# Performance work log

Measured on AMD Instinct MI355X. Metric: run time of the kernel, lower is better.

Reference implementation:

```python
import jax, jax.numpy as jnp
import numpy as np
from jax import lax

H = 39  # hidden size == input feature size (hardcoded in the torch module)


def _lstm_scan(xs, W_ih, W_hh, b_ih, b_hh):
    """Run a unidirectional LSTM over xs: (T, B, I) -> (T, B, H).
    PyTorch gate order: i, f, g, o."""
    T, B, _ = xs.shape
    # Precompute input projections for all timesteps: (T, B, 4H)
    pre = jnp.einsum('tbi,gi->tbg', xs, W_ih) + b_ih + b_hh
    h0 = jnp.zeros((B, H), dtype=xs.dtype)
    c0 = jnp.zeros((B, H), dtype=xs.dtype)

    def step(carry, g_in):
        h, c = carry
        g = g_in + h @ W_hh.T  # (B, 4H)
        i, f, gg, o = jnp.split(g, 4, axis=-1)
        i = jax.nn.sigmoid(i)
        f = jax.nn.sigmoid(f)
        gg = jnp.tanh(gg)
        o = jax.nn.sigmoid(o)
        c = f * c + i * gg
        h = o * jnp.tanh(c)
        return (h, c), h

    _, hs = lax.scan(step, (h0, c0), pre)
    return hs  # (T, B, H)


def setup_inputs() -> dict:
    key = jax.random.key(0)
    ks = jax.random.split(key, 9)
    B, T = 512, 2048
    s = 1.0 / np.sqrt(H)
    x = jax.random.normal(ks[0], (B, T * H), dtype=jnp.float32)
    def w(k, shape):
        return jax.random.uniform(k, shape, dtype=jnp.float32, minval=-s, maxval=s)
    return {
        'x': x,
        'W_ih_f': w(ks[1], (4 * H, H)),
        'W_hh_f': w(ks[2], (4 * H, H)),
        'b_ih_f': w(ks[3], (4 * H,)),
        'b_hh_f': w(ks[4], (4 * H,)),
        'W_ih_b': w(ks[5], (4 * H, H)),
        'W_hh_b': w(ks[6], (4 * H, H)),
        'b_ih_b': w(ks[7], (4 * H,)),
        'b_hh_b': w(ks[8], (4 * H,)),
    }


def reference(x, W_ih_f, W_hh_f, b_ih_f, b_hh_f, W_ih_b, W_hh_b, b_ih_b, b_hh_b):
    B = x.shape[0]
    T = x.shape[1] // H
    xs = jnp.swapaxes(x.reshape(B, T, H), 0, 1)  # (T, B, H)

    h_f = _lstm_scan(xs, W_ih_f, W_hh_f, b_ih_f, b_hh_f)          # forward dir, time order
    h_b_rev = _lstm_scan(xs[::-1], W_ih_b, W_hh_b, b_ih_b, b_hh_b)  # backward dir, processing order
    # torch output for backward dir is h_b_rev flipped to time order; the module then
    # flips it again along time before concat -> equals h_b_rev directly.
    out = jnp.concatenate([h_f, h_b_rev], axis=-1)  # (T, B, 2H)
    out = jnp.swapaxes(out, 0, 1).reshape(B, T * 2 * H)
    return out
```

## Files before the change

### kernel.cpp

```cpp
#include <hip/hip_runtime.h>
#include <math.h>

#define H   39
#define G4  156
#define TL  2048
#define BB  512

__device__ __forceinline__ float sigmoid_f(float x) {
    return 1.0f / (1.0f + __expf(-x));
}

__device__ __forceinline__ float tanh_f(float x) {
    float a = fabsf(x);
    float e = __expf(2.0f * a);
    float t = 1.0f - 2.0f / (e + 1.0f);
    return copysignf(t, x);
}

__global__ __launch_bounds__(192, 3)
void lstm_bidir_kernel(const float* __restrict__ x,
                       const float* __restrict__ W_ih_f, const float* __restrict__ W_hh_f,
                       const float* __restrict__ b_ih_f, const float* __restrict__ b_hh_f,
                       const float* __restrict__ W_ih_b, const float* __restrict__ W_hh_b,
                       const float* __restrict__ b_ih_b, const float* __restrict__ b_hh_b,
                       float* __restrict__ out)
{
    const int blk = blockIdx.x;
    const int b   = blk >> 1;
    const int dir = blk & 1;
    const int j   = threadIdx.x;

    const float* W_ih = dir ? W_ih_b : W_ih_f;
    const float* W_hh = dir ? W_hh_b : W_hh_f;
    const float* b_ih = dir ? b_ih_b : b_ih_f;
    const float* b_hh = dir ? b_hh_b : b_hh_f;

    __shared__ float h_buf[40];
    __shared__ float x_buf[40];
    __shared__ float gates[G4];

    float wih[H], whh[H];
    float bias = 0.0f;
    if (j < G4) {
        #pragma unroll
        for (int k = 0; k < H; ++k) {
            wih[k] = W_ih[j * H + k];
            whh[k] = W_hh[j * H + k];
        }
        bias = b_ih[j] + b_hh[j];
    }

    const float* xrow = x + (size_t)b * (TL * H);
    float* orow = out + (size_t)b * (TL * 2 * H) + dir * H;

    float c = 0.0f;
    if (j < H) {
        h_buf[j] = 0.0f;
        const int t0 = dir ? (TL - 1) : 0;
        x_buf[j] = xrow[t0 * H + j];
    }
    __syncthreads();

    for (int s = 0; s < TL; ++s) {
        float xnext = 0.0f;
        if (j < H && (s + 1) < TL) {
            const int tn = dir ? (TL - 2 - s) : (s + 1);
            xnext = xrow[tn * H + j];
        }

        if (j < G4) {
            float acc0 = bias, acc1 = 0.0f;
            #pragma unroll
            for (int k = 0; k < H; ++k) {
                acc0 = fmaf(wih[k], x_buf[k], acc0);
                acc1 = fmaf(whh[k], h_buf[k], acc1);
            }
            const float g = acc0 + acc1;
            const float act = (j >= 2 * H && j < 3 * H) ? tanh_f(g) : sigmoid_f(g);
            gates[j] = act;
        }
        __syncthreads();

        if (j < H) {
            const float ig = gates[j];
            const float fg = gates[H + j];
            const float gg = gates[2 * H + j];
            const float og = gates[3 * H + j];
            c = fmaf(fg, c, ig * gg);
            const float h = og * tanh_f(c);
            h_buf[j] = h;
            x_buf[j] = xnext;
            orow[(size_t)s * (2 * H) + j] = h;
        }
        __syncthreads();
    }
}

extern "C" void kernel_launch(void* const* d_in, const int* in_sizes, int n_in,
                              void* d_out, int out_size, void* d_ws, size_t ws_size,
                              hipStream_t stream) {
    const float* x      = (const float*)d_in[0];
    const float* W_ih_f = (const float*)d_in[1];
    const float* W_hh_f = (const float*)d_in[2];
    const float* b_ih_f = (const float*)d_in[3];
    const float* b_hh_f = (const float*)d_in[4];
    const float* W_ih_b = (const float*)d_in[5];
    const float* W_hh_b = (const float*)d_in[6];
    const float* b_ih_b = (const float*)d_in[7];
    const float* b_hh_b = (const float*)d_in[8];
    float* out = (float*)d_out;

    dim3 grid(BB * 2);
    dim3 block(192);
    lstm_bidir_kernel<<<grid, block, 0, stream>>>(
        x, W_ih_f, W_hh_f, b_ih_f, b_hh_f,
        W_ih_b, W_hh_b, b_ih_b, b_hh_b, out);
}
```

Baseline: 2.122 ms.

## Split each gate row across two lanes with float4 LDS reads and fused activations

Each gate row's dot product is now split between two threads, each holding half the weights as float4 registers and combining partial sums with a lane shuffle, and the block grows from 192 to 320 threads. Hidden and input vectors are read from shared memory as float4, and tanh/sigmoid use a single exp-plus-hardware-reciprocal formulation (tanh expressed as 2*sigmoid(2x)-1). The aim is to shorten the per-timestep serial dependency chain and cut LDS read instructions in this latency-bound recurrence. The cost is more waves per block, an extra shuffle per step, and an unclamped exp that can overflow for large negative arguments, though the reciprocal likely still yields the correct limit.

```diff
diff --git a/kernel.cpp b/kernel.cpp
--- a/kernel.cpp
+++ b/kernel.cpp
@@ -6,18 +6,7 @@
 #define TL  2048
 #define BB  512
 
-__device__ __forceinline__ float sigmoid_f(float x) {
-    return 1.0f / (1.0f + __expf(-x));
-}
-
-__device__ __forceinline__ float tanh_f(float x) {
-    float a = fabsf(x);
-    float e = __expf(2.0f * a);
-    float t = 1.0f - 2.0f / (e + 1.0f);
-    return copysignf(t, x);
-}
-
-__global__ __launch_bounds__(192, 3)
+__global__ __launch_bounds__(320, 5)
 void lstm_bidir_kernel(const float* __restrict__ x,
                        const float* __restrict__ W_ih_f, const float* __restrict__ W_hh_f,
                        const float* __restrict__ b_ih_f, const float* __restrict__ b_hh_f,
@@ -28,69 +17,96 @@
     const int blk = blockIdx.x;
     const int b   = blk >> 1;
     const int dir = blk & 1;
-    const int j   = threadIdx.x;
+    const int tid = threadIdx.x;
+    const int j   = tid >> 1;
+    const int p   = tid & 1;
+    const bool rowActive = (tid < 2 * G4);
 
-    const float* W_ih = dir ? W_ih_b : W_ih_f;
-    const float* W_hh = dir ? W_hh_b : W_hh_f;
-    const float* b_ih = dir ? b_ih_b : b_ih_f;
-    const float* b_hh = dir ? b_hh_b : b_hh_f;
+    const float* __restrict__ W_ih = dir ? W_ih_b : W_ih_f;
+    const float* __restrict__ W_hh = dir ? W_hh_b : W_hh_f;
+    const float* __restrict__ b_ih = dir ? b_ih_b : b_ih_f;
+    const float* __restrict__ b_hh = dir ? b_hh_b : b_hh_f;
 
-    __shared__ float h_buf[40];
-    __shared__ float x_buf[40];
+    __shared__ __align__(16) float xbf[40];
+    __shared__ __align__(16) float hbf[40];
     __shared__ float gates[G4];
+    float4* xb4 = (float4*)xbf;
+    float4* hb4 = (float4*)hbf;
 
-    float wih[H], whh[H];
+    float4 wih[5], whh[5];
     float bias = 0.0f;
-    if (j < G4) {
+    if (rowActive) {
         #pragma unroll
-        for (int k = 0; k < H; ++k) {
-            wih[k] = W_ih[j * H + k];
-            whh[k] = W_hh[j * H + k];
+        for (int m = 0; m < 5; ++m) {
+            const int k0 = 8 * m + 4 * p;
+            float a[4], h[4];
+            #pragma unroll
+            for (int e = 0; e < 4; ++e) {
+                const int k = k0 + e;
+                a[e] = (k < H) ? W_ih[j * H + k] : 0.0f;
+                h[e] = (k < H) ? W_hh[j * H + k] : 0.0f;
+            }
+            wih[m] = make_float4(a[0], a[1], a[2], a[3]);
+            whh[m] = make_float4(h[0], h[1], h[2], h[3]);
         }
         bias = b_ih[j] + b_hh[j];
     }
+    const bool  isg  = (j >= 2 * H) && (j < 3 * H);
+    const float amul = isg ? 2.0f : 1.0f;
+    const float aoff = isg ? -1.0f : 0.0f;
 
-    const float* xrow = x + (size_t)b * (TL * H);
-    float* orow = out + (size_t)b * (TL * 2 * H) + dir * H;
+    const float* __restrict__ xrow = x + (size_t)b * (TL * H);
+    float* __restrict__ orow = out + (size_t)b * (TL * 2 * H) + dir * H;
 
     float c = 0.0f;
-    if (j < H) {
-        h_buf[j] = 0.0f;
+    if (tid < 40) {
+        hbf[tid] = 0.0f;
         const int t0 = dir ? (TL - 1) : 0;
-        x_buf[j] = xrow[t0 * H + j];
+        xbf[tid] = (tid < H) ? xrow[(size_t)t0 * H + tid] : 0.0f;
     }
     __syncthreads();
 
     for (int s = 0; s < TL; ++s) {
         float xnext = 0.0f;
-        if (j < H && (s + 1) < TL) {
+        if (tid < H && (s + 1) < TL) {
             const int tn = dir ? (TL - 2 - s) : (s + 1);
-            xnext = xrow[tn * H + j];
+            xnext = xrow[(size_t)tn * H + tid];
         }
 
-        if (j < G4) {
-            float acc0 = bias, acc1 = 0.0f;
+        if (rowActive) {
+            float4 acc = make_float4(0.0f, 0.0f, 0.0f, 0.0f);
             #pragma unroll
-            for (int k = 0; k < H; ++k) {
-                acc0 = fmaf(wih[k], x_buf[k], acc0);
-                acc1 = fmaf(whh[k], h_buf[k], acc1);
+            for (int m = 0; m < 5; ++m) {
+                const int ci = 2 * m + p;
+                const float4 xv = xb4[ci];
+                const float4 hv = hb4[ci];
+                acc.x = fmaf(wih[m].x, xv.x, fmaf(whh[m].x, hv.x, acc.x));
+                acc.y = fmaf(wih[m].y, xv.y, fmaf(whh[m].y, hv.y, acc.y));
+                acc.z = fmaf(wih[m].z, xv.z, fmaf(whh[m].z, hv.z, acc.z));
+                acc.w = fmaf(wih[m].w, xv.w, fmaf(whh[m].w, hv.w, acc.w));
             }
-            const float g = acc0 + acc1;
-            const float act = (j >= 2 * H && j < 3 * H) ? tanh_f(g) : sigmoid_f(g);
-            gates[j] = act;
+            float psum = (acc.x + acc.y) + (acc.z + acc.w);
+            const float tot  = psum + __shfl_xor(psum, 1) + bias;
+            const float targ = amul * tot;
+            const float e    = __expf(-targ);
+            const float sg   = __builtin_amdgcn_rcpf(1.0f + e);
+            const float act  = fmaf(amul, sg, aoff);
+            if (p == 0) gates[j] = act;
         }
         __syncthreads();
 
-        if (j < H) {
-            const float ig = gates[j];
-            const float fg = gates[H + j];
-            const float gg = gates[2 * H + j];
-            const float og = gates[3 * H + j];
+        if (tid < H) {
+            const float ig = gates[tid];
+            const float fg = gates[H + tid];
+            const float gg = gates[2 * H + tid];
+            const float og = gates[3 * H + tid];
             c = fmaf(fg, c, ig * gg);
-            const float h = og * tanh_f(c);
-            h_buf[j] = h;
-            x_buf[j] = xnext;
-            orow[(size_t)s * (2 * H) + j] = h;
+            const float e2 = __expf(-2.0f * c);
+            const float th = fmaf(2.0f, __builtin_amdgcn_rcpf(1.0f + e2), -1.0f);
+            const float h  = og * th;
+            hbf[tid] = h;
+            xbf[tid] = xnext;
+            orow[(size_t)s * (2 * H) + tid] = h;
         }
         __syncthreads();
     }
@@ -111,7 +127,7 @@
     float* out = (float*)d_out;
 
     dim3 grid(BB * 2);
-    dim3 block(192);
+    dim3 block(320);
     lstm_bidir_kernel<<<grid, block, 0, stream>>>(
         x, W_ih_f, W_hh_f, b_ih_f, b_hh_f,
         W_ih_b, W_hh_b, b_ih_b, b_hh_b, out);
```

Measured after the change: 1.907 ms. 10.1% less time.
